# Optimization experiments

Hardware: AMD Instinct MI355X
Metric: run time of the kernel (lower is better)

The kernel has to match this reference:

```python
import jax, jax.numpy as jnp
import numpy as np

HIDDEN = 256
N_PROT = 12288
N_MOL = 6144
N_BATCH = 32


def setup_inputs() -> dict:
    key = jax.random.key(0)
    ks = jax.random.split(key, 10)
    s = 1.0 / np.sqrt(HIDDEN)  # torch Linear default init scale
    inp = {
        "prot_embed": jax.random.normal(ks[0], (N_PROT, HIDDEN), jnp.float32),
        "mol_embed": jax.random.normal(ks[1], (N_MOL, HIDDEN), jnp.float32),
        "prot_batch": jnp.sort(jax.random.randint(ks[2], (N_PROT,), 0, N_BATCH)),
        "mol_batch": jnp.sort(jax.random.randint(ks[3], (N_MOL,), 0, N_BATCH)),
        "Wq": jax.random.uniform(ks[4], (HIDDEN, HIDDEN), jnp.float32, -s, s),
        "bq": jax.random.uniform(ks[5], (HIDDEN,), jnp.float32, -s, s),
        "Wk": jax.random.uniform(ks[6], (HIDDEN, HIDDEN), jnp.float32, -s, s),
        "bk": jax.random.uniform(ks[7], (HIDDEN,), jnp.float32, -s, s),
        "Wv": jax.random.uniform(ks[8], (HIDDEN, HIDDEN), jnp.float32, -s, s),
        "bv": jax.random.uniform(ks[9], (HIDDEN,), jnp.float32, -s, s),
    }
    return inp


def reference(prot_embed, mol_embed, prot_batch, mol_batch, Wq, bq, Wk, bk, Wv, bv):
    # Linear projections (torch nn.Linear: x @ W.T + b)
    Q = prot_embed @ Wq.T + bq            # [N, H]
    K = mol_embed @ Wk.T + bk             # [M, H]
    V = mol_embed @ Wv.T + bv             # [M, H]

    scale = 1.0 / jnp.sqrt(jnp.asarray(Q.shape[-1], Q.dtype))
    scores = (Q @ K.T) * scale            # [N, M]

    # block mask: same-batch pairs only
    mask = prot_batch[:, None] == mol_batch[None, :]   # [N, M] bool
    neg_inf = jnp.asarray(-jnp.inf, scores.dtype)
    scores = jnp.where(mask, scores, neg_inf)

    # stable masked softmax; rows with no valid key -> all zeros
    # (matches torch softmax(-inf row) -> nan -> nan_to_num(0.0))
    row_any = mask.any(axis=-1, keepdims=True)
    mx = jnp.max(scores, axis=-1, keepdims=True)
    mx = jnp.where(row_any, mx, 0.0)
    e = jnp.exp(scores - mx)              # exp(-inf)=0 on masked entries
    denom = jnp.sum(e, axis=-1, keepdims=True)
    attn = e / jnp.where(row_any, denom, 1.0)  # [N, M]

    out = attn @ V                        # [N, H]
    return out, attn
```

## Files before the change

### kernel.cpp

```cpp
#include <hip/hip_runtime.h>

#define NPROT 12288
#define NMOL  6144
#define HID   256
#define NB    32

#define WQ_O   4718592
#define WK_O   4784128
#define WV_O   4849664
#define BQ_O   4915200
#define BK_O   4915456
#define BV_O   4915712
#define Q_O    4915968
#define K_O    8061696
#define VT_O   9634560
#define END_O  11207424

typedef __attribute__((ext_vector_type(4))) float f32x4;
typedef __attribute__((ext_vector_type(8))) short bf16x8;
typedef unsigned short u16;
typedef unsigned int   u32;

__device__ __forceinline__ float b2f(u16 u){
  union { u32 i; float f; } v; v.i = ((u32)u) << 16; return v.f;
}
__device__ __forceinline__ u16 f2b(float f){
  union { float fl; u32 i; } v; v.fl = f;
  u32 i = v.i;
  return (u16)((i + 0x7FFFu + ((i >> 16) & 1u)) >> 16);
}

__global__ __launch_bounds__(256) void prep_kernel(
    const float* __restrict__ Wq, const float* __restrict__ Wk,
    const float* __restrict__ Wv, const float* __restrict__ bq,
    const float* __restrict__ bk, const float* __restrict__ bv,
    const int* __restrict__ pb, const int* __restrict__ mb,
    int* __restrict__ rg, u16* __restrict__ cvt)
{
  int g = blockIdx.x * 256 + threadIdx.x;
  const float* src = nullptr; u16* dst = nullptr; int off = 0;
  if      (g < 16384) { src = Wq; dst = cvt + WQ_O; off = g; }
  else if (g < 32768) { src = Wk; dst = cvt + WK_O; off = g - 16384; }
  else if (g < 49152) { src = Wv; dst = cvt + WV_O; off = g - 32768; }
  else if (g < 49216) { src = bq; dst = cvt + BQ_O; off = g - 49152; }
  else if (g < 49280) { src = bk; dst = cvt + BK_O; off = g - 49216; }
  else if (g < 49344) { src = bv; dst = cvt + BV_O; off = g - 49280; }
  if (src){
    f32x4 v = *(const f32x4*)(src + (size_t)off * 4);
    ushort4 o;
    o.x = f2b(v[0]); o.y = f2b(v[1]); o.z = f2b(v[2]); o.w = f2b(v[3]);
    *(ushort4*)(dst + (size_t)off * 4) = o;
  }

  if (blockIdx.x == 0 && threadIdx.x < 64){
    int t = threadIdx.x;
    const int* arr = (t < 32) ? pb : mb;
    int n          = (t < 32) ? NPROT : NMOL;
    int target     = (t & 31) + 1;
    int lo = 0, hi = n;
    while (lo < hi){
      int mid = (lo + hi) >> 1;
      if (arr[mid] < target) lo = mid + 1; else hi = mid;
    }
    int end = lo;
    int prev = __shfl(end, t - 1);
    int start = ((t & 31) == 0) ? 0 : prev;
    int b = t & 31;
    if (t < 32){ rg[b] = start; rg[32 + b] = end; }
    else       { rg[64 + b] = start; rg[96 + b] = end; }
  }
}

__global__ __launch_bounds__(256) void proj_kernel(
    const float* __restrict__ prot, const float* __restrict__ mol,
    const u16* __restrict__ cvt,
    u16* __restrict__ Q, u16* __restrict__ K, u16* __restrict__ Vt)
{
  __shared__ u16 xlds[16][264];
  __shared__ u16 tlds[4][64][18];
  int rb = blockIdx.x;
  int proj;
  const float* X; const u16 *W, *B;
  if      (rb < 768) { proj = 0; X = prot; W = cvt + WQ_O; B = cvt + BQ_O; }
  else if (rb < 1152){ proj = 1; rb -= 768;  X = mol; W = cvt + WK_O; B = cvt + BK_O; }
  else               { proj = 2; rb -= 1152; X = mol; W = cvt + WV_O; B = cvt + BV_O; }
  int rowbase = rb * 16;

  {
    int r  = threadIdx.x >> 4;
    int c0 = (threadIdx.x & 15) * 16;
    const float* xp = X + (size_t)(rowbase + r) * HID + c0;
    f32x4 v0 = *(const f32x4*)(xp);
    f32x4 v1 = *(const f32x4*)(xp + 4);
    f32x4 v2 = *(const f32x4*)(xp + 8);
    f32x4 v3 = *(const f32x4*)(xp + 12);
    u16* d = &xlds[r][c0];
    ushort4 o0, o1, o2, o3;
    o0.x = f2b(v0[0]); o0.y = f2b(v0[1]); o0.z = f2b(v0[2]); o0.w = f2b(v0[3]);
    o1.x = f2b(v1[0]); o1.y = f2b(v1[1]); o1.z = f2b(v1[2]); o1.w = f2b(v1[3]);
    o2.x = f2b(v2[0]); o2.y = f2b(v2[1]); o2.z = f2b(v2[2]); o2.w = f2b(v2[3]);
    o3.x = f2b(v3[0]); o3.y = f2b(v3[1]); o3.z = f2b(v3[2]); o3.w = f2b(v3[3]);
    *(ushort4*)(d)      = o0;
    *(ushort4*)(d + 4)  = o1;
    *(ushort4*)(d + 8)  = o2;
    *(ushort4*)(d + 12) = o3;
  }
  __syncthreads();

  int wave = threadIdx.x >> 6, lane = threadIdx.x & 63;
  int m = lane & 15, q = lane >> 4;
  int colbase = wave * 64;

  f32x4 acc[4] = {};
  for (int k0 = 0; k0 < HID; k0 += 32){
    bf16x8 a = *(const bf16x8*)(&xlds[m][k0 + q*8]);
    #pragma unroll
    for (int ct = 0; ct < 4; ct++){
      bf16x8 b = *(const bf16x8*)(W + (size_t)(colbase + ct*16 + m) * HID + k0 + q*8);
      acc[ct] = __builtin_amdgcn_mfma_f32_16x16x32_bf16(a, b, acc[ct], 0, 0, 0);
    }
  }

  if (proj < 2){
    u16* O = (proj == 0) ? Q : K;
    #pragma unroll
    for (int ct = 0; ct < 4; ct++){
      int col = colbase + ct*16 + m;
      float bb = b2f(B[col]);
      #pragma unroll
      for (int r = 0; r < 4; r++){
        int row = rowbase + q*4 + r;
        O[(size_t)row * HID + col] = f2b(acc[ct][r] + bb);
      }
    }
  } else {
    #pragma unroll
    for (int ct = 0; ct < 4; ct++){
      int lc = ct*16 + m;
      float bb = b2f(B[colbase + lc]);
      #pragma unroll
      for (int r = 0; r < 4; r++)
        tlds[wave][lc][q*4 + r] = f2b(acc[ct][r] + bb);
    }
    __syncthreads();
    int col = colbase + lane;
    u32 packed[8];
    #pragma unroll
    for (int i = 0; i < 8; i++){
      u16 lo = tlds[wave][lane][2*i];
      u16 hi = tlds[wave][lane][2*i+1];
      packed[i] = (u32)lo | ((u32)hi << 16);
    }
    u16* dst = Vt + (size_t)col * NMOL + rowbase;
    uint4 v0 = {packed[0], packed[1], packed[2], packed[3]};
    uint4 v1 = {packed[4], packed[5], packed[6], packed[7]};
    *(uint4*)dst = v0;
    *(uint4*)(dst + 8) = v1;
  }
}

__global__ __launch_bounds__(256) void attn_kernel(
    const int* __restrict__ rg,
    const u16* __restrict__ Q, const u16* __restrict__ K,
    const u16* __restrict__ Vt, float* __restrict__ dout)
{
  __shared__ u16 P[16][392];
  __shared__ float mxw[4][16];
  __shared__ float smw[4][16];
  const float scale = 0.0625f;
  float* outf  = dout;
  float* attnf = dout + (size_t)NPROT * HID;

  int b = blockIdx.y;
  int ps = rg[b], pe = rg[32+b], ms = rg[64+b], me = rg[96+b];
  int Np = pe - ps, Nm = me - ms;
  if (Np <= 0) return;

  int wave = threadIdx.x >> 6, lane = threadIdx.x & 63;
  int m = lane & 15, q = lane >> 4;
  int ntiles = (Np + 15) >> 4;

  int bs = 0, ce = 0;
  if (Nm > 0){ bs = ms & ~31; ce = bs + ((me - bs + 31) & ~31); }

  for (int tile = blockIdx.x; tile < ntiles; tile += 32){
    int row0 = ps + tile * 16;
    int qr = min(row0 + m, NPROT - 1);
    const u16* qrow = Q + (size_t)qr * HID;
    bf16x8 qf[8];
    #pragma unroll
    for (int kk = 0; kk < 8; kk++)
      qf[kk] = *(const bf16x8*)(qrow + kk*32 + q*8);

    if (Nm > 0){
      int myj0 = bs + wave * 16;
      f32x4 sreg[6];
      float mx[4] = {-1e30f, -1e30f, -1e30f, -1e30f};
      #pragma unroll
      for (int c = 0; c < 6; c++){
        int j0 = myj0 + 64*c;
        if (j0 < ce){
          int col = j0 + m;
          bool valid = (col >= ms) && (col < me);
          const u16* krow = K + (size_t)col * HID;
          f32x4 s0 = {0.f,0.f,0.f,0.f}, s1 = {0.f,0.f,0.f,0.f};
          #pragma unroll
          for (int kk = 0; kk < 4; kk++){
            bf16x8 kb0 = *(const bf16x8*)(krow + kk*32 + q*8);
            bf16x8 kb1 = *(const bf16x8*)(krow + (kk+4)*32 + q*8);
            s0 = __builtin_amdgcn_mfma_f32_16x16x32_bf16(qf[kk],   kb0, s0, 0, 0, 0);
            s1 = __builtin_amdgcn_mfma_f32_16x16x32_bf16(qf[kk+4], kb1, s1, 0, 0, 0);
          }
          f32x4 sv;
          #pragma unroll
          for (int r = 0; r < 4; r++)
            sv[r] = valid ? (s0[r] + s1[r]) * scale : -1e30f;
          sreg[c] = sv;
          float cm[4];
          #pragma unroll
          for (int r = 0; r < 4; r++) cm[r] = sv[r];
          #pragma unroll
          for (int d = 1; d < 16; d <<= 1)
            #pragma unroll
            for (int r = 0; r < 4; r++)
              cm[r] = fmaxf(cm[r], __shfl_xor(cm[r], d, 16));
          #pragma unroll
          for (int r = 0; r < 4; r++) mx[r] = fmaxf(mx[r], cm[r]);
        }
      }
      if (m == 0){
        #pragma unroll
        for (int r = 0; r < 4; r++) mxw[wave][q*4 + r] = mx[r];
      }
      __syncthreads();
      float gmx[4];
      #pragma unroll
      for (int r = 0; r < 4; r++){
        int row = q*4 + r;
        float M = mxw[0][row];
        #pragma unroll
        for (int w = 1; w < 4; w++) M = fmaxf(M, mxw[w][row]);
        gmx[r] = M;
      }

      float sm[4] = {0.f, 0.f, 0.f, 0.f};
      #pragma unroll
      for (int c = 0; c < 6; c++){
        int j0 = myj0 + 64*c;
        if (j0 < ce){
          f32x4 e;
          #pragma unroll
          for (int r = 0; r < 4; r++) e[r] = __expf(sreg[c][r] - gmx[r]);
          sreg[c] = e;
          float t[4];
          #pragma unroll
          for (int r = 0; r < 4; r++) t[r] = e[r];
          #pragma unroll
          for (int d = 1; d < 16; d <<= 1)
            #pragma unroll
            for (int r = 0; r < 4; r++)
              t[r] += __shfl_xor(t[r], d, 16);
          #pragma unroll
          for (int r = 0; r < 4; r++) sm[r] += t[r];
        }
      }
      if (m == 0){
        #pragma unroll
        for (int r = 0; r < 4; r++) smw[wave][q*4 + r] = sm[r];
      }
      __syncthreads();
      float ginv[4];
      #pragma unroll
      for (int r = 0; r < 4; r++){
        int row = q*4 + r;
        float S = smw[0][row] + smw[1][row] + smw[2][row] + smw[3][row];
        ginv[r] = (S > 0.f) ? (1.f / S) : 0.f;
      }

      #pragma unroll
      for (int c = 0; c < 6; c++){
        int j0 = myj0 + 64*c;
        if (j0 < ce){
          int col = j0 + m;
          int jl = j0 - bs;
          bool valid = (col >= ms) && (col < me);
          #pragma unroll
          for (int r = 0; r < 4; r++){
            float p = sreg[c][r] * ginv[r];
            P[q*4 + r][jl + m] = f2b(p);
            int row = row0 + q*4 + r;
            if (valid && row < pe)
              __builtin_nontemporal_store(p, attnf + (size_t)row * NMOL + col);
          }
        }
      }
      __syncthreads();

      f32x4 oacc[4] = {};
      for (int j0 = bs; j0 < ce; j0 += 32){
        int jl = j0 - bs;
        bf16x8 a = *(const bf16x8*)(&P[m][jl + q*8]);
        #pragma unroll
        for (int c2 = 0; c2 < 4; c2++){
          int ct = wave*4 + c2;
          bf16x8 vb = *(const bf16x8*)(Vt + (size_t)(ct*16 + m) * NMOL + j0 + q*8);
          oacc[c2] = __builtin_amdgcn_mfma_f32_16x16x32_bf16(a, vb, oacc[c2], 0, 0, 0);
        }
      }
      #pragma unroll
      for (int c2 = 0; c2 < 4; c2++){
        int col = (wave*4 + c2)*16 + m;
        #pragma unroll
        for (int r = 0; r < 4; r++){
          int row = row0 + q*4 + r;
          if (row < pe) outf[(size_t)row * HID + col] = oacc[c2][r];
        }
      }
    } else {
      #pragma unroll
      for (int c2 = 0; c2 < 4; c2++){
        int col = (wave*4 + c2)*16 + m;
        #pragma unroll
        for (int r = 0; r < 4; r++){
          int row = row0 + q*4 + r;
          if (row < pe) outf[(size_t)row * HID + col] = 0.f;
        }
      }
    }
    __syncthreads();
  }
}

extern "C" void kernel_launch(void* const* d_in, const int* in_sizes, int n_in,
                              void* d_out, int out_size, void* d_ws, size_t ws_size,
                              hipStream_t stream)
{
  (void)in_sizes; (void)n_in; (void)out_size;
  const float* prot = (const float*)d_in[0];
  const float* mol  = (const float*)d_in[1];
  const int* pb     = (const int*)d_in[2];
  const int* mb     = (const int*)d_in[3];
  const float* Wq   = (const float*)d_in[4];
  const float* bq   = (const float*)d_in[5];
  const float* Wk   = (const float*)d_in[6];
  const float* bk   = (const float*)d_in[7];
  const float* Wv   = (const float*)d_in[8];
  const float* bv   = (const float*)d_in[9];

  const size_t need = 1024 + (size_t)END_O * 2;
  if (ws_size < need) return;

  char* ws = (char*)d_ws;
  int* rg  = (int*)ws;
  u16* cvt = (u16*)(ws + 1024);
  u16* Qp  = cvt + Q_O;
  u16* Kp  = cvt + K_O;
  u16* Vtp = cvt + VT_O;
  float* out = (float*)d_out;

  hipMemsetAsync(out + (size_t)NPROT * HID, 0,
                 (size_t)NPROT * NMOL * sizeof(float), stream);

  prep_kernel<<<dim3(193), dim3(256), 0, stream>>>(
      Wq, Wk, Wv, bq, bk, bv, pb, mb, rg, cvt);
  proj_kernel<<<dim3(1536), dim3(256), 0, stream>>>(
      prot, mol, cvt, Qp, Kp, Vtp);
  attn_kernel<<<dim3(32, NB), dim3(256), 0, stream>>>(rg, Qp, Kp, Vtp, out);
}
```

Measured before the change: 404.7 us.

## Fuse weight prep, attn zero-fill and projection into a single kernel

Drops the separate prep kernel and the hipMemsetAsync over the whole attention matrix. The projection kernel now converts fp32 weights to bf16 on the fly, and interleaved odd blocks zero-fill the attention output with nontemporal stores. A final block computes the batch ranges. This saves two launches and overlaps the large zero-fill with projection compute, at the cost of redundant per-block weight conversion and fp32 weight loads.

```diff
diff --git a/kernel.cpp b/kernel.cpp
--- a/kernel.cpp
+++ b/kernel.cpp
@@ -5,85 +5,72 @@
 #define HID   256
 #define NB    32
 
-#define WQ_O   4718592
-#define WK_O   4784128
-#define WV_O   4849664
-#define BQ_O   4915200
-#define BK_O   4915456
-#define BV_O   4915712
-#define Q_O    4915968
-#define K_O    8061696
-#define VT_O   9634560
-#define END_O  11207424
+#define FROWS_BLK 49152
 
 typedef __attribute__((ext_vector_type(4))) float f32x4;
 typedef __attribute__((ext_vector_type(8))) short bf16x8;
 typedef unsigned short u16;
 typedef unsigned int   u32;
 
-__device__ __forceinline__ float b2f(u16 u){
-  union { u32 i; float f; } v; v.i = ((u32)u) << 16; return v.f;
-}
 __device__ __forceinline__ u16 f2b(float f){
   union { float fl; u32 i; } v; v.fl = f;
   u32 i = v.i;
   return (u16)((i + 0x7FFFu + ((i >> 16) & 1u)) >> 16);
 }
 
-__global__ __launch_bounds__(256) void prep_kernel(
-    const float* __restrict__ Wq, const float* __restrict__ Wk,
-    const float* __restrict__ Wv, const float* __restrict__ bq,
-    const float* __restrict__ bk, const float* __restrict__ bv,
+__device__ __forceinline__ void fill_rows8(float* attnf, int fid){
+  float* dst = attnf + (size_t)fid * FROWS_BLK + threadIdx.x * 4;
+  f32x4 z = {0.f, 0.f, 0.f, 0.f};
+  #pragma unroll 4
+  for (int i = 0; i < 48; i++)
+    __builtin_nontemporal_store(z, (f32x4*)(dst + i * 1024));
+}
+
+__global__ __launch_bounds__(256) void proj_fill_kernel(
+    const float* __restrict__ prot, const float* __restrict__ mol,
+    const float* __restrict__ Wq, const float* __restrict__ bq,
+    const float* __restrict__ Wk, const float* __restrict__ bk,
+    const float* __restrict__ Wv, const float* __restrict__ bv,
     const int* __restrict__ pb, const int* __restrict__ mb,
-    int* __restrict__ rg, u16* __restrict__ cvt)
-{
-  int g = blockIdx.x * 256 + threadIdx.x;
-  const float* src = nullptr; u16* dst = nullptr; int off = 0;
-  if      (g < 16384) { src = Wq; dst = cvt + WQ_O; off = g; }
-  else if (g < 32768) { src = Wk; dst = cvt + WK_O; off = g - 16384; }
-  else if (g < 49152) { src = Wv; dst = cvt + WV_O; off = g - 32768; }
-  else if (g < 49216) { src = bq; dst = cvt + BQ_O; off = g - 49152; }
-  else if (g < 49280) { src = bk; dst = cvt + BK_O; off = g - 49216; }
-  else if (g < 49344) { src = bv; dst = cvt + BV_O; off = g - 49280; }
-  if (src){
-    f32x4 v = *(const f32x4*)(src + (size_t)off * 4);
-    ushort4 o;
-    o.x = f2b(v[0]); o.y = f2b(v[1]); o.z = f2b(v[2]); o.w = f2b(v[3]);
-    *(ushort4*)(dst + (size_t)off * 4) = o;
-  }
-
-  if (blockIdx.x == 0 && threadIdx.x < 64){
-    int t = threadIdx.x;
-    const int* arr = (t < 32) ? pb : mb;
-    int n          = (t < 32) ? NPROT : NMOL;
-    int target     = (t & 31) + 1;
-    int lo = 0, hi = n;
-    while (lo < hi){
-      int mid = (lo + hi) >> 1;
-      if (arr[mid] < target) lo = mid + 1; else hi = mid;
-    }
-    int end = lo;
-    int prev = __shfl(end, t - 1);
-    int start = ((t & 31) == 0) ? 0 : prev;
-    int b = t & 31;
-    if (t < 32){ rg[b] = start; rg[32 + b] = end; }
-    else       { rg[64 + b] = start; rg[96 + b] = end; }
-  }
-}
-
-__global__ __launch_bounds__(256) void proj_kernel(
-    const float* __restrict__ prot, const float* __restrict__ mol,
-    const u16* __restrict__ cvt,
-    u16* __restrict__ Q, u16* __restrict__ K, u16* __restrict__ Vt)
+    int* __restrict__ rg,
+    u16* __restrict__ Q, u16* __restrict__ K, u16* __restrict__ Vt,
+    float* __restrict__ dout)
 {
   __shared__ u16 xlds[16][264];
   __shared__ u16 tlds[4][64][18];
-  int rb = blockIdx.x;
+
+  int blk = blockIdx.x;
+  if (blk >= 3072){
+    if (threadIdx.x < 64){
+      int t = threadIdx.x;
+      const int* arr = (t < 32) ? pb : mb;
+      int n          = (t < 32) ? NPROT : NMOL;
+      int target     = (t & 31) + 1;
+      int lo = 0, hi = n;
+      while (lo < hi){
+        int mid = (lo + hi) >> 1;
+        if (arr[mid] < target) lo = mid + 1; else hi = mid;
+      }
+      int end = lo;
+      int prev = __shfl(end, t - 1);
+      int start = ((t & 31) == 0) ? 0 : prev;
+      int bb = t & 31;
+      if (t < 32){ rg[bb] = start; rg[32 + bb] = end; }
+      else       { rg[64 + bb] = start; rg[96 + bb] = end; }
+    }
+    return;
+  }
+  if (blk & 1){
+    fill_rows8(dout + (size_t)NPROT * HID, blk >> 1);
+    return;
+  }
+
+  int rb = blk >> 1;
   int proj;
-  const float* X; const u16 *W, *B;
-  if      (rb < 768) { proj = 0; X = prot; W = cvt + WQ_O; B = cvt + BQ_O; }
-  else if (rb < 1152){ proj = 1; rb -= 768;  X = mol; W = cvt + WK_O; B = cvt + BK_O; }
-  else               { proj = 2; rb -= 1152; X = mol; W = cvt + WV_O; B = cvt + BV_O; }
+  const float *X, *W, *B;
+  if      (rb < 768) { proj = 0; X = prot; W = Wq; B = bq; }
+  else if (rb < 1152){ proj = 1; rb -= 768;  X = mol; W = Wk; B = bk; }
+  else               { proj = 2; rb -= 1152; X = mol; W = Wv; B = bv; }
   int rowbase = rb * 16;
 
   {
@@ -116,8 +103,16 @@
     bf16x8 a = *(const bf16x8*)(&xlds[m][k0 + q*8]);
     #pragma unroll
     for (int ct = 0; ct < 4; ct++){
-      bf16x8 b = *(const bf16x8*)(W + (size_t)(colbase + ct*16 + m) * HID + k0 + q*8);
-      acc[ct] = __builtin_amdgcn_mfma_f32_16x16x32_bf16(a, b, acc[ct], 0, 0, 0);
+      const float* wrow = W + (size_t)(colbase + ct*16 + m) * HID + k0 + q*8;
+      f32x4 w0 = *(const f32x4*)(wrow);
+      f32x4 w1 = *(const f32x4*)(wrow + 4);
+      bf16x8 bfr;
+      #pragma unroll
+      for (int i = 0; i < 4; i++){
+        bfr[i]     = (short)f2b(w0[i]);
+        bfr[4 + i] = (short)f2b(w1[i]);
+      }
+      acc[ct] = __builtin_amdgcn_mfma_f32_16x16x32_bf16(a, bfr, acc[ct], 0, 0, 0);
     }
   }
 
@@ -126,7 +121,7 @@
     #pragma unroll
     for (int ct = 0; ct < 4; ct++){
       int col = colbase + ct*16 + m;
-      float bb = b2f(B[col]);
+      float bb = B[col];
       #pragma unroll
       for (int r = 0; r < 4; r++){
         int row = rowbase + q*4 + r;
@@ -137,7 +132,7 @@
     #pragma unroll
     for (int ct = 0; ct < 4; ct++){
       int lc = ct*16 + m;
-      float bb = b2f(B[colbase + lc]);
+      float bb = B[colbase + lc];
       #pragma unroll
       for (int r = 0; r < 4; r++)
         tlds[wave][lc][q*4 + r] = f2b(acc[ct][r] + bb);
@@ -347,23 +342,17 @@
   const float* Wv   = (const float*)d_in[8];
   const float* bv   = (const float*)d_in[9];
 
-  const size_t need = 1024 + (size_t)END_O * 2;
+  const size_t need = 1024 + (size_t)(NPROT + 2*NMOL) * HID * 2;
   if (ws_size < need) return;
 
   char* ws = (char*)d_ws;
   int* rg  = (int*)ws;
-  u16* cvt = (u16*)(ws + 1024);
-  u16* Qp  = cvt + Q_O;
-  u16* Kp  = cvt + K_O;
-  u16* Vtp = cvt + VT_O;
+  u16* Qp  = (u16*)(ws + 1024);
+  u16* Kp  = Qp + (size_t)NPROT * HID;
+  u16* Vtp = Kp + (size_t)NMOL * HID;
   float* out = (float*)d_out;
 
-  hipMemsetAsync(out + (size_t)NPROT * HID, 0,
-                 (size_t)NPROT * NMOL * sizeof(float), stream);
-
-  prep_kernel<<<dim3(193), dim3(256), 0, stream>>>(
-      Wq, Wk, Wv, bq, bk, bv, pb, mb, rg, cvt);
-  proj_kernel<<<dim3(1536), dim3(256), 0, stream>>>(
-      prot, mol, cvt, Qp, Kp, Vtp);
+  proj_fill_kernel<<<dim3(3073), dim3(256), 0, stream>>>(
+      prot, mol, Wq, bq, Wk, bk, Wv, bv, pb, mb, rg, Qp, Kp, Vtp, out);
   attn_kernel<<<dim3(32, NB), dim3(256), 0, stream>>>(rg, Qp, Kp, Vtp, out);
 }
```

Result: slower. 430.8 us (+6.4%).
